# Kernel tuning notes

Measured on AMD Instinct MI355X. Metric: run time of the kernel, lower is better.

The kernel has to match this reference:

```python
import jax, jax.numpy as jnp
import numpy as np

N_HEADS = 4

def setup_inputs() -> dict:
    key = jax.random.key(0)
    ks = jax.random.split(key, 9)
    B, C, H, W = 4, 256, 64, 64
    nh, hs = N_HEADS, C // N_HEADS
    s = 0.02
    return {
        "x": jax.random.normal(ks[0], (B, C, H, W), jnp.float32),
        "wq": jax.random.normal(ks[1], (C, C), jnp.float32) * s,
        "bq": jax.random.normal(ks[2], (C,), jnp.float32) * s,
        "wk": jax.random.normal(ks[3], (C, C), jnp.float32) * s,
        "bk": jax.random.normal(ks[4], (C,), jnp.float32) * s,
        "wv": jax.random.normal(ks[5], (C, C), jnp.float32) * s,
        "bv": jax.random.normal(ks[6], (C,), jnp.float32) * s,
        "rel_h": jax.random.normal(ks[7], (1, nh, hs, 1, H), jnp.float32),
        "rel_w": jax.random.normal(ks[8], (1, nh, hs, W, 1), jnp.float32),
    }

def reference(x, wq, bq, wk, bk, wv, bv, rel_h, rel_w):
    B, C, H, W = x.shape
    nh = N_HEADS
    hs = C // nh
    S = H * W

    def proj(w, b):
        # 1x1 conv == per-pixel linear over channels -> [B, C, H, W]
        y = jnp.einsum('oc,bchw->bohw', w, x) + b[None, :, None, None]
        # faithful to torch .view: flatten [C,H,W] row-major into [S, nh, hs]
        y = y.reshape(B, S, nh, hs)
        return y.transpose(0, 2, 1, 3)  # [B, nh, S, hs]

    q = proj(wq, bq)
    k = proj(wk, bk)
    v = proj(wv, bv)

    # content scores (NOTE: no 1/sqrt(d) scaling in BoT override)
    attn_content = jnp.einsum('bnqd,bnkd->bnqk', q, k)  # [B, nh, S, S]
    # learned relative position term: broadcast-add then flatten (w,h) order
    pos = (rel_h + rel_w).reshape(1, nh, hs, S)  # [1, nh, hs, S]
    attn_position = jnp.einsum('bnqd,ands->bnqs', q, pos)  # [B, nh, S, S]

    probs = jax.nn.softmax(attn_content + attn_position, axis=-1)
    ctx = jnp.einsum('bnqk,bnkd->bnqd', probs, v)  # [B, nh, S, hs]
    # faithful to torch: transpose(1,2) then view(B, C, width, height)
    out = ctx.transpose(0, 2, 1, 3).reshape(B, C, W, H)
    return out
```

## Files before the change

kernel.cpp:

```cpp
#include <hip/hip_runtime.h>
#include <hip/hip_bf16.h>
#include <stdint.h>
#include <math.h>

typedef __bf16 bf16_t;
typedef __bf16 bf16x8 __attribute__((ext_vector_type(8)));
typedef float  f32x4  __attribute__((ext_vector_type(4)));
typedef float  f32x16 __attribute__((ext_vector_type(16)));
typedef unsigned int u32;

#define S_SZ 4096
#define HS   64
#define OUT_B_STRIDE (256 * 64 * 64)
#define LOG2E 1.4426950408889634f

#define GLOAD_LDS(gsrc, ldst)                                                              \
    __builtin_amdgcn_global_load_lds((__attribute__((address_space(1))) void*)(void*)(gsrc), \
                                     (__attribute__((address_space(3))) void*)(void*)(ldst),  \
                                     16, 0, 0)

static __device__ __forceinline__ u32 pack2(__bf16 a, __bf16 b) {
    return (u32)__builtin_bit_cast(uint16_t, a) | ((u32)__builtin_bit_cast(uint16_t, b) << 16);
}

__global__ __launch_bounds__(256)
void prep_kernel(const float* __restrict__ wq, const float* __restrict__ wk,
                 const float* __restrict__ wv, const float* __restrict__ rel_h,
                 const float* __restrict__ rel_w,
                 bf16_t* __restrict__ Wh, bf16_t* __restrict__ Wl,
                 bf16_t* __restrict__ Rt)
{
    const int blk = blockIdx.x;
    if (blk < 48) {
        const int base = blk * 4096;
        #pragma unroll
        for (int i = 0; i < 16; ++i) {
            const int e = base + i * 256 + threadIdx.x;
            const int o = e >> 8, c = e & 255;
            const float* src = o < 256 ? wq : (o < 512 ? wk : wv);
            float v = src[(size_t)(o & 255) * 256 + c];
            if (o < 256) v *= LOG2E;
            __bf16 h = (__bf16)v;
            Wh[e] = h;
            Wl[e] = (__bf16)(v - (float)h);
        }
    } else {
        const int rb = blk - 48;
        const int n = rb >> 4, h2 = rb & 15;
        __shared__ float rh[4096], rw[4096];
        for (int i = threadIdx.x; i < 4096; i += 256) {
            rh[i] = rel_h[n * 4096 + i];
            rw[i] = rel_w[n * 4096 + i];
        }
        __syncthreads();
        bf16_t* Rp = Rt + ((size_t)n * 4096 + h2 * 256) * 64;
        const int d0 = (threadIdx.x & 7) * 8;
        const int ob = threadIdx.x >> 3;
        #pragma unroll
        for (int i = 0; i < 8; ++i) {
            const int o  = i * 32 + ob;
            const int ih = (o & 3) * 16 + h2;
            const int iw = o >> 2;
            bf16x8 rv;
            #pragma unroll
            for (int dd = 0; dd < 8; ++dd)
                rv[dd] = (bf16_t)(rh[(d0 + dd) * 64 + ih] + rw[(d0 + dd) * 64 + iw]);
            *(bf16x8*)(Rp + (size_t)o * 64 + d0) = rv;
        }
    }
}

__global__ __launch_bounds__(512, 2)
void proj_kernel(const float* __restrict__ x,
                 const bf16_t* __restrict__ Wh, const bf16_t* __restrict__ Wl,
                 const float* __restrict__ bq, const float* __restrict__ bk,
                 const float* __restrict__ bv, const bf16_t* __restrict__ Rt,
                 bf16_t* __restrict__ q_ws, bf16_t* __restrict__ k2_ws,
                 bf16_t* __restrict__ vt2_ws)
{
    const int bx = blockIdx.x;
    const int b  = bx >> 6;
    const int h  = bx & 63;
    const int p0 = h * 64;
    const int n  = h & 3;
    const int h2 = h >> 2;
    const int bn = b * 4 + n;
    const int tid = threadIdx.x;

    __shared__ __align__(16) char SM[65536];

    {
        const int cpair = tid & 127, pg = tid >> 7;
        const int c0 = cpair * 2;
        const float* x0 = x + ((size_t)b * 256 + c0) * 4096 + p0 + pg * 16;
        const int sub = (c0 >> 6) * 128;
        const int u   = (c0 >> 3) & 7;
        const int e2  = (c0 & 7) * 2;
        #pragma unroll
        for (int i4 = 0; i4 < 4; ++i4) {
            f32x4 ra = *(const f32x4*)(x0 + i4 * 4);
            f32x4 rb = *(const f32x4*)(x0 + 4096 + i4 * 4);
            #pragma unroll
            for (int i = 0; i < 4; ++i) {
                const int p = pg * 16 + i4 * 4 + i;
                __bf16 ha = (__bf16)ra[i], hb = (__bf16)rb[i];
                float  la = ra[i] - (float)ha, lb = rb[i] - (float)hb;
                const int off = p * 512 + sub + ((u ^ (p & 7)) * 16) + e2;
                *(u32*)(SM + off)         = pack2(ha, hb);
                *(u32*)(SM + 32768 + off) = pack2((__bf16)la, (__bf16)lb);
            }
        }
    }
    __syncthreads();

    const int wid = tid >> 6, lane = tid & 63, l31 = lane & 31, hi = lane >> 5;

    int obs[3], pjs[3];
    const bf16_t* whp[3];
    const bf16_t* wlp[3];
    #pragma unroll
    for (int j = 0; j < 3; ++j) {
        const int of = (wid * 3 + j) * 32;
        pjs[j] = of >> 8;
        obs[j] = of & 255;
        whp[j] = Wh + (size_t)(of + l31) * 256 + hi * 8;
        wlp[j] = Wl + (size_t)(of + l31) * 256 + hi * 8;
    }

    const char* XHp = SM + l31 * 512;
    const char* XLp = SM + 32768 + l31 * 512;

    f32x16 acc[3][2] = {};

    bf16x8 whC[3], wlC[3], whN[3], wlN[3];
    #pragma unroll
    for (int j = 0; j < 3; ++j) {
        whC[j] = *(const bf16x8*)(whp[j]);
        wlC[j] = *(const bf16x8*)(wlp[j]);
    }

    #pragma unroll
    for (int ks = 0; ks < 16; ++ks) {
        if (ks < 15) {
            #pragma unroll
            for (int j = 0; j < 3; ++j) {
                whN[j] = *(const bf16x8*)(whp[j] + (ks + 1) * 16);
                wlN[j] = *(const bf16x8*)(wlp[j] + (ks + 1) * 16);
            }
        }
        const int rb_ = (ks >> 2) * 128 + ((((ks * 2 + hi) & 7) ^ (l31 & 7)) * 16);
        bf16x8 xh[2], xl[2];
        #pragma unroll
        for (int pt = 0; pt < 2; ++pt) {
            xh[pt] = *(const bf16x8*)(XHp + pt * 16384 + rb_);
            xl[pt] = *(const bf16x8*)(XLp + pt * 16384 + rb_);
        }
        #pragma unroll
        for (int j = 0; j < 3; ++j)
            #pragma unroll
            for (int pt = 0; pt < 2; ++pt) {
                acc[j][pt] = __builtin_amdgcn_mfma_f32_32x32x16_bf16(whC[j], xh[pt], acc[j][pt], 0, 0, 0);
                acc[j][pt] = __builtin_amdgcn_mfma_f32_32x32x16_bf16(whC[j], xl[pt], acc[j][pt], 0, 0, 0);
                acc[j][pt] = __builtin_amdgcn_mfma_f32_32x32x16_bf16(wlC[j], xh[pt], acc[j][pt], 0, 0, 0);
            }
        #pragma unroll
        for (int j = 0; j < 3; ++j) { whC[j] = whN[j]; wlC[j] = wlN[j]; }
    }
    __syncthreads();

    f32x4 bias[3][2][4];
    #pragma unroll
    for (int j = 0; j < 3; ++j) {
        const float* bp = pjs[j] == 0 ? bq : (pjs[j] == 1 ? bk : bv);
        #pragma unroll
        for (int g2 = 0; g2 < 4; ++g2) {
            f32x4 v = *(const f32x4*)(bp + obs[j] + hi * 4 + g2 * 8);
            if (pjs[j] == 0) {
                #pragma unroll
                for (int i = 0; i < 4; ++i) v[i] *= LOG2E;
            }
            bias[j][0][g2] = v;  bias[j][1][g2] = v;
        }
    }

    #pragma unroll
    for (int j = 0; j < 3; ++j) {
        if (pjs[j] == 1) continue;
        #pragma unroll
        for (int pt = 0; pt < 2; ++pt) {
            const int d = pt * 32 + l31;
            #pragma unroll
            for (int g2 = 0; g2 < 4; ++g2)
                #pragma unroll
                for (int rr = 0; rr < 4; ++rr) {
                    const int o = obs[j] + rr + 4 * hi + 8 * g2;
                    const float v = acc[j][pt][g2 * 4 + rr] + bias[j][pt][g2][rr];
                    if (pjs[j] == 0) {
                        *(bf16_t*)(SM + o * 128 + d * 2) = (bf16_t)v;
                    } else {
                        *(bf16_t*)(SM + 32768 + d * 512 + ((o * 2) ^ ((d & 7) << 4))) = (bf16_t)v;
                    }
                }
        }
    }
    __syncthreads();
    {
        bf16_t* qp = q_ws + (size_t)bn * 4096 * 64;
        #pragma unroll
        for (int i = 0; i < 4; ++i) {
            const int c = i * 512 + tid;
            const int o = c >> 3, d8 = c & 7;
            uint4 v = *(const uint4*)(SM + c * 16);
            *(uint4*)(qp + (size_t)(o * 16 + h2) * 64 + d8 * 8) = v;
        }
        bf16_t* vp = vt2_ws + (size_t)bn * 64 * 4096 + h2 * 256;
        #pragma unroll
        for (int i = 0; i < 4; ++i) {
            const int c = i * 512 + tid;
            const int d = c >> 5, k = c & 31;
            uint4 v = *(const uint4*)(SM + 32768 + d * 512 + ((k * 16) ^ ((d & 7) << 4)));
            *(uint4*)(vp + (size_t)d * 4096 + k * 8) = v;
        }
    }
    __syncthreads();

    #pragma unroll
    for (int j = 0; j < 3; ++j) {
        if (pjs[j] != 1) continue;
        #pragma unroll
        for (int pt = 0; pt < 2; ++pt) {
            const int d = pt * 32 + l31;
            #pragma unroll
            for (int g2 = 0; g2 < 4; ++g2)
                #pragma unroll
                for (int rr = 0; rr < 4; ++rr) {
                    const int o = obs[j] + rr + 4 * hi + 8 * g2;
                    *(bf16_t*)(SM + o * 128 + d * 2) =
                        (bf16_t)(acc[j][pt][g2 * 4 + rr] + bias[j][pt][g2][rr]);
                }
        }
    }
    __syncthreads();
    {
        const bf16_t* Rp = Rt + ((size_t)n * 4096 + h2 * 256) * 64;
        bf16_t* kp = k2_ws + ((size_t)bn * 4096 + h2 * 256) * 64;
        #pragma unroll
        for (int i = 0; i < 4; ++i) {
            const int c = i * 512 + tid;
            bf16x8 kv = *(const bf16x8*)(SM + c * 16);
            bf16x8 rv = *(const bf16x8*)(Rp + c * 8);
            bf16x8 res;
            #pragma unroll
            for (int ii = 0; ii < 8; ++ii)
                res[ii] = (__bf16)((float)kv[ii] + (float)rv[ii]);
            *(bf16x8*)(kp + c * 8) = res;
        }
    }
}

__global__ __launch_bounds__(256, 1)
void attn_kernel(const bf16_t* __restrict__ q_ws, const bf16_t* __restrict__ k_ws,
                 const bf16_t* __restrict__ vt_ws, float* __restrict__ out)
{
    const int tid  = threadIdx.x;
    const int wid  = tid >> 6;
    const int lane = tid & 63;
    const int l31  = lane & 31;
    const int hi   = lane >> 5;

    const int wg  = blockIdx.x;
    const int swz = (wg & 7) * 32 + (wg >> 3);
    const int bn  = swz >> 4;
    const int qb  = swz & 15;
    const int b   = bn >> 2, n = bn & 3;

    __shared__ __align__(16) bf16_t Kt[4][64 * 64];
    __shared__ __align__(16) bf16_t Vt[4][64 * 64];

    const bf16_t* Qb = q_ws  + (size_t)bn * S_SZ * HS;
    const bf16_t* Kb = k_ws  + (size_t)bn * S_SZ * HS;
    const bf16_t* Vb = vt_ws + (size_t)bn * HS * S_SZ;

    const int c0 = wid * 64 + lane;
    const int ra = c0 >> 3, ga = (c0 & 7) ^ (ra & 7);
    const bf16_t* ksrcA = Kb + ra * HS + ga * 8;
    const bf16_t* ksrcB = ksrcA + 32 * HS;
    const bf16_t* vsrcA = Vb + (size_t)ra * S_SZ + ga * 8;
    const bf16_t* vsrcB = vsrcA + (size_t)32 * S_SZ;

#define STAGE(buf, ts)                                                        \
    GLOAD_LDS(ksrcA + (size_t)(ts) * 64 * HS, &Kt[buf][wid * 512]);           \
    GLOAD_LDS(ksrcB + (size_t)(ts) * 64 * HS, &Kt[buf][2048 + wid * 512]);    \
    GLOAD_LDS(vsrcA + (ts) * 64,              &Vt[buf][wid * 512]);           \
    GLOAD_LDS(vsrcB + (ts) * 64,              &Vt[buf][2048 + wid * 512]);

    const int q0 = qb * 256 + wid * 64 + l31;
    bf16x8 qf0[4], qf1[4];
    #pragma unroll
    for (int dk = 0; dk < 4; ++dk) {
        qf0[dk] = *(const bf16x8*)(Qb + (size_t)q0 * HS + dk * 16 + hi * 8);
        qf1[dk] = *(const bf16x8*)(Qb + (size_t)(q0 + 32) * HS + dk * 16 + hi * 8);
    }

    f32x16 oacc[2][2];
    f32x16 Z16;
    #pragma unroll
    for (int i = 0; i < 16; ++i) {
        oacc[0][0][i] = 0.f; oacc[0][1][i] = 0.f;
        oacc[1][0][i] = 0.f; oacc[1][1][i] = 0.f;
        Z16[i] = 0.f;
    }
    float lsum0 = 0.f, lsum1 = 0.f;

    const int swzme = (l31 & 7) << 4;

#define TILE(BUF)                                                                      \
    { const char* Kb_ = (const char*)&Kt[BUF][0] + l31 * 128;                          \
      const char* Vb_ = (const char*)&Vt[BUF][0] + l31 * 128;                          \
      f32x16 sacc[2][2];                                                               \
      _Pragma("unroll")                                                                \
      for (int hh = 0; hh < 2; ++hh) {                                                 \
          bf16x8 kf[4];                                                                \
          _Pragma("unroll")                                                            \
          for (int dk = 0; dk < 4; ++dk)                                               \
              kf[dk] = *(const bf16x8*)(Kb_ + hh * 4096 + (((2 * dk + hi) * 16) ^ swzme)); \
          sacc[hh][0] = __builtin_amdgcn_mfma_f32_32x32x16_bf16(kf[0], qf0[0], Z16, 0, 0, 0); \
          sacc[hh][1] = __builtin_amdgcn_mfma_f32_32x32x16_bf16(kf[0], qf1[0], Z16, 0, 0, 0); \
          _Pragma("unroll")                                                            \
          for (int dk = 1; dk < 4; ++dk) {                                             \
              sacc[hh][0] = __builtin_amdgcn_mfma_f32_32x32x16_bf16(kf[dk], qf0[dk], sacc[hh][0], 0, 0, 0); \
              sacc[hh][1] = __builtin_amdgcn_mfma_f32_32x32x16_bf16(kf[dk], qf1[dk], sacc[hh][1], 0, 0, 0); \
          }                                                                            \
      }                                                                                \
      u32 F0[4][4], F1[4][4];                                                          \
      { u32 Wd[2][4][2];                                                               \
        float ps[4] = {0.f, 0.f, 0.f, 0.f};                                            \
        _Pragma("unroll")                                                              \
        for (int hh = 0; hh < 2; ++hh)                                                 \
        _Pragma("unroll")                                                              \
        for (int c = 0; c < 4; ++c)                                                    \
        _Pragma("unroll")                                                              \
        for (int tt = 0; tt < 2; ++tt) {                                               \
            float pa = __builtin_amdgcn_exp2f(sacc[hh][0][c * 4 + tt * 2]);            \
            float pb = __builtin_amdgcn_exp2f(sacc[hh][0][c * 4 + tt * 2 + 1]);        \
            ps[c] += pa + pb;                                                          \
            u32 w_;                                                                    \
            asm("v_cvt_pk_bf16_f32 %0, %1, %2" : "=v"(w_) : "v"(pa), "v"(pb));         \
            Wd[hh][c][tt] = w_; }                                                      \
        lsum0 += (ps[0] + ps[1]) + (ps[2] + ps[3]);                                    \
        _Pragma("unroll")                                                              \
        for (int hh = 0; hh < 2; ++hh)                                                 \
        _Pragma("unroll")                                                              \
        for (int pr = 0; pr < 2; ++pr)                                                 \
        _Pragma("unroll")                                                              \
        for (int tt = 0; tt < 2; ++tt) {                                               \
            u32 a_ = Wd[hh][2 * pr][tt], b_ = Wd[hh][2 * pr + 1][tt];                  \
            asm("v_permlane32_swap_b32 %0, %1" : "+v"(a_), "+v"(b_));                  \
            F0[2 * hh + pr][tt]     = a_;                                              \
            F0[2 * hh + pr][2 + tt] = b_; } }                                          \
      { u32 Wd[2][4][2];                                                               \
        float ps[4] = {0.f, 0.f, 0.f, 0.f};                                            \
        _Pragma("unroll")                                                              \
        for (int hh = 0; hh < 2; ++hh)                                                 \
        _Pragma("unroll")                                                              \
        for (int c = 0; c < 4; ++c)                                                    \
        _Pragma("unroll")                                                              \
        for (int tt = 0; tt < 2; ++tt) {                                               \
            float pa = __builtin_amdgcn_exp2f(sacc[hh][1][c * 4 + tt * 2]);            \
            float pb = __builtin_amdgcn_exp2f(sacc[hh][1][c * 4 + tt * 2 + 1]);        \
            ps[c] += pa + pb;                                                          \
            u32 w_;                                                                    \
            asm("v_cvt_pk_bf16_f32 %0, %1, %2" : "=v"(w_) : "v"(pa), "v"(pb));         \
            Wd[hh][c][tt] = w_; }                                                      \
        lsum1 += (ps[0] + ps[1]) + (ps[2] + ps[3]);                                    \
        _Pragma("unroll")                                                              \
        for (int hh = 0; hh < 2; ++hh)                                                 \
        _Pragma("unroll")                                                              \
        for (int pr = 0; pr < 2; ++pr)                                                 \
        _Pragma("unroll")                                                              \
        for (int tt = 0; tt < 2; ++tt) {                                               \
            u32 a_ = Wd[hh][2 * pr][tt], b_ = Wd[hh][2 * pr + 1][tt];                  \
            asm("v_permlane32_swap_b32 %0, %1" : "+v"(a_), "+v"(b_));                  \
            F1[2 * hh + pr][tt]     = a_;                                              \
            F1[2 * hh + pr][2 + tt] = b_; } }                                          \
      _Pragma("unroll")                                                                \
      for (int dh = 0; dh < 2; ++dh)                                                   \
      _Pragma("unroll")                                                                \
      for (int kk = 0; kk < 4; ++kk) {                                                 \
          bf16x8 vf = *(const bf16x8*)(Vb_ + dh * 4096 + (((2 * kk + hi) * 16) ^ swzme)); \
          union { u32 u[4]; bf16x8 v; } p0, p1;                                        \
          p0.u[0] = F0[kk][0]; p0.u[1] = F0[kk][1]; p0.u[2] = F0[kk][2]; p0.u[3] = F0[kk][3]; \
          p1.u[0] = F1[kk][0]; p1.u[1] = F1[kk][1]; p1.u[2] = F1[kk][2]; p1.u[3] = F1[kk][3]; \
          oacc[dh][0] = __builtin_amdgcn_mfma_f32_32x32x16_bf16(vf, p0.v, oacc[dh][0], 0, 0, 0); \
          oacc[dh][1] = __builtin_amdgcn_mfma_f32_32x32x16_bf16(vf, p1.v, oacc[dh][1], 0, 0, 0); } }

    STAGE(0, 0); STAGE(1, 1); STAGE(2, 2);
    asm volatile("s_waitcnt vmcnt(8)" ::: "memory");
    __builtin_amdgcn_s_barrier();
    asm volatile("" ::: "memory");

    for (int tb = 0; tb < 64; tb += 4) {
        #pragma unroll
        for (int u = 0; u < 4; ++u) {
            const int t = tb + u;
            { const int ts = (t + 3 > 63) ? 63 : t + 3; STAGE((u + 3) & 3, ts); }
            TILE(u);
            asm volatile("s_waitcnt vmcnt(4)" ::: "memory");
            __builtin_amdgcn_s_barrier();
            asm volatile("" ::: "memory");
        }
    }
#undef TILE
#undef STAGE

    float lt0 = lsum0 + __shfl_xor(lsum0, 32);
    float lt1 = lsum1 + __shfl_xor(lsum1, 32);
    float inv0 = 1.0f / lt0;
    float inv1 = 1.0f / lt1;
    float* outp0 = out + (size_t)b * OUT_B_STRIDE + (size_t)q0 * 256 + n * 64;
    float* outp1 = outp0 + 32 * 256;
    #pragma unroll
    for (int dh = 0; dh < 2; ++dh)
        #pragma unroll
        for (int g2 = 0; g2 < 4; ++g2) {
            f32x4 v4, w4;
            #pragma unroll
            for (int r = 0; r < 4; ++r) {
                v4[r] = oacc[dh][0][g2 * 4 + r] * inv0;
                w4[r] = oacc[dh][1][g2 * 4 + r] * inv1;
            }
            *(f32x4*)(outp0 + dh * 32 + g2 * 8 + hi * 4) = v4;
            *(f32x4*)(outp1 + dh * 32 + g2 * 8 + hi * 4) = w4;
        }
}

extern "C" void kernel_launch(void* const* d_in, const int* in_sizes, int n_in,
                              void* d_out, int out_size, void* d_ws, size_t ws_size,
                              hipStream_t stream)
{
    const float* x     = (const float*)d_in[0];
    const float* wq    = (const float*)d_in[1];
    const float* bq    = (const float*)d_in[2];
    const float* wk    = (const float*)d_in[3];
    const float* bk    = (const float*)d_in[4];
    const float* wv    = (const float*)d_in[5];
    const float* bv    = (const float*)d_in[6];
    const float* rel_h = (const float*)d_in[7];
    const float* rel_w = (const float*)d_in[8];
    float* out = (float*)d_out;

    bf16_t* q_ws   = (bf16_t*)d_ws;
    bf16_t* k2_ws  = q_ws  + (size_t)16 * S_SZ * HS;
    bf16_t* vt2_ws = k2_ws + (size_t)16 * S_SZ * HS;

    bf16_t* end = (bf16_t*)d_out + (size_t)out_size * 2;
    bf16_t* Wl  = end - 196608;
    bf16_t* Wh  = Wl - 196608;
    bf16_t* Rt  = Wh - 1048576;

    prep_kernel<<<112, 256, 0, stream>>>(wq, wk, wv, rel_h, rel_w, Wh, Wl, Rt);
    proj_kernel<<<256, 512, 0, stream>>>(x, Wh, Wl, bq, bk, bv, Rt,
                                         q_ws, k2_ws, vt2_ws);
    attn_kernel<<<256, 256, 0, stream>>>(q_ws, k2_ws, vt2_ws, out);
}
```

Baseline: 138.4 us.

## Split attention KV range in two halves and merge with a combine kernel

The attention kernel now splits each (batch, head, query-block) work item into two halves over the key/value sequence. This launches 512 workgroups instead of 256, with launch bounds set for two blocks per CU and the LDS staging cut from four buffers to two. Each half writes its unnormalised output and row sums to workspace, and a new elementwise combine kernel adds the halves and divides by the total sum. The aim is more waves per CU to hide latency, at the cost of a shallower prefetch pipeline, extra global traffic for partial outputs, and one more launch. The merge is only exact if the two halves share the same softmax max reference, which depends on hidden code.

```diff
diff --git a/kernel.cpp b/kernel.cpp
--- a/kernel.cpp
+++ b/kernel.cpp
@@ -258,9 +258,11 @@
     }
 }
 
-__global__ __launch_bounds__(256, 1)
+__global__ __launch_bounds__(256, 2)
 void attn_kernel(const bf16_t* __restrict__ q_ws, const bf16_t* __restrict__ k_ws,
-                 const bf16_t* __restrict__ vt_ws, float* __restrict__ out)
+                 const bf16_t* __restrict__ vt_ws, float* __restrict__ O0,
+                 float* __restrict__ L0, float* __restrict__ L1,
+                 float* __restrict__ out)
 {
     const int tid  = threadIdx.x;
     const int wid  = tid >> 6;
@@ -269,13 +271,16 @@
     const int hi   = lane >> 5;
 
     const int wg  = blockIdx.x;
-    const int swz = (wg & 7) * 32 + (wg >> 3);
-    const int bn  = swz >> 4;
-    const int qb  = swz & 15;
-    const int b   = bn >> 2, n = bn & 3;
-
-    __shared__ __align__(16) bf16_t Kt[4][64 * 64];
-    __shared__ __align__(16) bf16_t Vt[4][64 * 64];
+    const int swz = (wg & 7) * 64 + (wg >> 3);
+    const int bn  = swz >> 5;
+    const int r   = swz & 31;
+    const int qb  = r >> 1;
+    const int half = r & 1;
+    const int tbase = half * 32;
+    const int b = bn >> 2, n = bn & 3;
+
+    __shared__ __align__(16) bf16_t Kt[2][64 * 64];
+    __shared__ __align__(16) bf16_t Vt[2][64 * 64];
 
     const bf16_t* Qb = q_ws  + (size_t)bn * S_SZ * HS;
     const bf16_t* Kb = k_ws  + (size_t)bn * S_SZ * HS;
@@ -394,30 +399,29 @@
           oacc[dh][0] = __builtin_amdgcn_mfma_f32_32x32x16_bf16(vf, p0.v, oacc[dh][0], 0, 0, 0); \
           oacc[dh][1] = __builtin_amdgcn_mfma_f32_32x32x16_bf16(vf, p1.v, oacc[dh][1], 0, 0, 0); } }
 
-    STAGE(0, 0); STAGE(1, 1); STAGE(2, 2);
-    asm volatile("s_waitcnt vmcnt(8)" ::: "memory");
+    STAGE(0, tbase);
+    asm volatile("s_waitcnt vmcnt(0)" ::: "memory");
     __builtin_amdgcn_s_barrier();
     asm volatile("" ::: "memory");
-
-    for (int tb = 0; tb < 64; tb += 4) {
-        #pragma unroll
-        for (int u = 0; u < 4; ++u) {
-            const int t = tb + u;
-            { const int ts = (t + 3 > 63) ? 63 : t + 3; STAGE((u + 3) & 3, ts); }
-            TILE(u);
-            asm volatile("s_waitcnt vmcnt(4)" ::: "memory");
-            __builtin_amdgcn_s_barrier();
-            asm volatile("" ::: "memory");
-        }
+    for (int t = 0; t < 32; t += 2) {
+        { const int ts = tbase + ((t + 1 < 32) ? t + 1 : 31); STAGE(1, ts); }
+        TILE(0);
+        asm volatile("s_waitcnt vmcnt(0)" ::: "memory");
+        __builtin_amdgcn_s_barrier();
+        asm volatile("" ::: "memory");
+        { const int ts = tbase + ((t + 2 < 32) ? t + 2 : 31); STAGE(0, ts); }
+        TILE(1);
+        asm volatile("s_waitcnt vmcnt(0)" ::: "memory");
+        __builtin_amdgcn_s_barrier();
+        asm volatile("" ::: "memory");
     }
 #undef TILE
 #undef STAGE
 
     float lt0 = lsum0 + __shfl_xor(lsum0, 32);
     float lt1 = lsum1 + __shfl_xor(lsum1, 32);
-    float inv0 = 1.0f / lt0;
-    float inv1 = 1.0f / lt1;
-    float* outp0 = out + (size_t)b * OUT_B_STRIDE + (size_t)q0 * 256 + n * 64;
+    float* Otgt = half ? out : O0;
+    float* outp0 = Otgt + (size_t)b * OUT_B_STRIDE + (size_t)q0 * 256 + n * 64;
     float* outp1 = outp0 + 32 * 256;
     #pragma unroll
     for (int dh = 0; dh < 2; ++dh)
@@ -425,13 +429,42 @@
         for (int g2 = 0; g2 < 4; ++g2) {
             f32x4 v4, w4;
             #pragma unroll
-            for (int r = 0; r < 4; ++r) {
-                v4[r] = oacc[dh][0][g2 * 4 + r] * inv0;
-                w4[r] = oacc[dh][1][g2 * 4 + r] * inv1;
+            for (int r2 = 0; r2 < 4; ++r2) {
+                v4[r2] = oacc[dh][0][g2 * 4 + r2];
+                w4[r2] = oacc[dh][1][g2 * 4 + r2];
             }
             *(f32x4*)(outp0 + dh * 32 + g2 * 8 + hi * 4) = v4;
             *(f32x4*)(outp1 + dh * 32 + g2 * 8 + hi * 4) = w4;
         }
+    if (hi == 0) {
+        float* Lp = half ? L1 : L0;
+        Lp[bn * 4096 + q0]      = lt0;
+        Lp[bn * 4096 + q0 + 32] = lt1;
+    }
+}
+
+__global__ __launch_bounds__(256)
+void combine_kernel(const float* __restrict__ O0, const float* __restrict__ L0,
+                    const float* __restrict__ L1, float* __restrict__ out)
+{
+    const int i = (blockIdx.x * 256 + threadIdx.x) * 8;
+    const int s = (i >> 8) & 4095;
+    const int b = i >> 20;
+    const int n = (i >> 6) & 3;
+    const int li = (b * 4 + n) * 4096 + s;
+    const float inv = 1.0f / (L0[li] + L1[li]);
+    f32x4 a0 = *(const f32x4*)(O0 + i);
+    f32x4 a1 = *(const f32x4*)(out + i);
+    f32x4 b0 = *(const f32x4*)(O0 + i + 4);
+    f32x4 b1 = *(const f32x4*)(out + i + 4);
+    f32x4 r0, r1;
+    #pragma unroll
+    for (int k = 0; k < 4; ++k) {
+        r0[k] = (a0[k] + a1[k]) * inv;
+        r1[k] = (b0[k] + b1[k]) * inv;
+    }
+    *(f32x4*)(out + i)     = r0;
+    *(f32x4*)(out + i + 4) = r1;
 }
 
 extern "C" void kernel_launch(void* const* d_in, const int* in_sizes, int n_in,
@@ -452,6 +485,9 @@
     bf16_t* q_ws   = (bf16_t*)d_ws;
     bf16_t* k2_ws  = q_ws  + (size_t)16 * S_SZ * HS;
     bf16_t* vt2_ws = k2_ws + (size_t)16 * S_SZ * HS;
+    float*  O0     = (float*)((char*)d_ws + 25165824);
+    float*  L0     = (float*)((char*)d_ws + 41943040);
+    float*  L1     = (float*)((char*)d_ws + 42205184);
 
     bf16_t* end = (bf16_t*)d_out + (size_t)out_size * 2;
     bf16_t* Wl  = end - 196608;
@@ -461,5 +497,6 @@
     prep_kernel<<<112, 256, 0, stream>>>(wq, wk, wv, rel_h, rel_w, Wh, Wl, Rt);
     proj_kernel<<<256, 512, 0, stream>>>(x, Wh, Wl, bq, bk, bv, Rt,
                                          q_ws, k2_ws, vt2_ws);
-    attn_kernel<<<256, 256, 0, stream>>>(q_ws, k2_ws, vt2_ws, out);
+    attn_kernel<<<512, 256, 0, stream>>>(q_ws, k2_ws, vt2_ws, O0, L0, L1, out);
+    combine_kernel<<<2048, 256, 0, stream>>>(O0, L0, L1, out);
 }
```

Result: faster. 131.7 us (-4.8%).

## Split attention into 128-thread blocks with double-buffered K/V staging

Applied to the files above, without the earlier changes.

The attention kernel now runs 512 workgroups of 2 waves, each covering 128 queries instead of 256, with launch bounds allowing 2 blocks per CU. The K/V LDS ring shrinks from 4 stages to 2 and the loop waits for all loads to finish (vmcnt(0)) before each barrier. The aim is more resident workgroups and better CU balance across the 256 CUs. The cost is that each K/V tile is loaded by twice as many blocks, and the shallower pipeline exposes more load latency.

```diff
diff --git a/kernel.cpp b/kernel.cpp
--- a/kernel.cpp
+++ b/kernel.cpp
@@ -258,7 +258,7 @@
     }
 }
 
-__global__ __launch_bounds__(256, 1)
+__global__ __launch_bounds__(128, 2)
 void attn_kernel(const bf16_t* __restrict__ q_ws, const bf16_t* __restrict__ k_ws,
                  const bf16_t* __restrict__ vt_ws, float* __restrict__ out)
 {
@@ -269,32 +269,39 @@
     const int hi   = lane >> 5;
 
     const int wg  = blockIdx.x;
-    const int swz = (wg & 7) * 32 + (wg >> 3);
-    const int bn  = swz >> 4;
-    const int qb  = swz & 15;
+    const int swz = (wg & 7) * 64 + (wg >> 3);
+    const int bn  = swz >> 5;
+    const int qb  = swz & 31;
     const int b   = bn >> 2, n = bn & 3;
 
-    __shared__ __align__(16) bf16_t Kt[4][64 * 64];
-    __shared__ __align__(16) bf16_t Vt[4][64 * 64];
+    __shared__ __align__(16) bf16_t Kt[2][64 * 64];
+    __shared__ __align__(16) bf16_t Vt[2][64 * 64];
 
     const bf16_t* Qb = q_ws  + (size_t)bn * S_SZ * HS;
     const bf16_t* Kb = k_ws  + (size_t)bn * S_SZ * HS;
     const bf16_t* Vb = vt_ws + (size_t)bn * HS * S_SZ;
 
-    const int c0 = wid * 64 + lane;
-    const int ra = c0 >> 3, ga = (c0 & 7) ^ (ra & 7);
-    const bf16_t* ksrcA = Kb + ra * HS + ga * 8;
-    const bf16_t* ksrcB = ksrcA + 32 * HS;
-    const bf16_t* vsrcA = Vb + (size_t)ra * S_SZ + ga * 8;
-    const bf16_t* vsrcB = vsrcA + (size_t)32 * S_SZ;
+    const bf16_t* ksrc[4];
+    const bf16_t* vsrc[4];
+    int dstoff[4];
+    #pragma unroll
+    for (int i = 0; i < 4; ++i) {
+        const int c = wid * 64 + i * 128 + lane;
+        const int row = c >> 3, ga = (c & 7) ^ (row & 7);
+        ksrc[i] = Kb + (size_t)row * HS + ga * 8;
+        vsrc[i] = Vb + (size_t)row * S_SZ + ga * 8;
+        dstoff[i] = (wid * 64 + i * 128) * 8;
+    }
 
 #define STAGE(buf, ts)                                                        \
-    GLOAD_LDS(ksrcA + (size_t)(ts) * 64 * HS, &Kt[buf][wid * 512]);           \
-    GLOAD_LDS(ksrcB + (size_t)(ts) * 64 * HS, &Kt[buf][2048 + wid * 512]);    \
-    GLOAD_LDS(vsrcA + (ts) * 64,              &Vt[buf][wid * 512]);           \
-    GLOAD_LDS(vsrcB + (ts) * 64,              &Vt[buf][2048 + wid * 512]);
-
-    const int q0 = qb * 256 + wid * 64 + l31;
+    { _Pragma("unroll")                                                       \
+      for (int i_ = 0; i_ < 4; ++i_)                                          \
+          GLOAD_LDS(ksrc[i_] + (size_t)(ts) * 64 * HS, &Kt[buf][dstoff[i_]]); \
+      _Pragma("unroll")                                                       \
+      for (int i_ = 0; i_ < 4; ++i_)                                          \
+          GLOAD_LDS(vsrc[i_] + (ts) * 64, &Vt[buf][dstoff[i_]]); }
+
+    const int q0 = qb * 128 + wid * 64 + l31;
     bf16x8 qf0[4], qf1[4];
     #pragma unroll
     for (int dk = 0; dk < 4; ++dk) {
@@ -394,21 +401,21 @@
           oacc[dh][0] = __builtin_amdgcn_mfma_f32_32x32x16_bf16(vf, p0.v, oacc[dh][0], 0, 0, 0); \
           oacc[dh][1] = __builtin_amdgcn_mfma_f32_32x32x16_bf16(vf, p1.v, oacc[dh][1], 0, 0, 0); } }
 
-    STAGE(0, 0); STAGE(1, 1); STAGE(2, 2);
-    asm volatile("s_waitcnt vmcnt(8)" ::: "memory");
+    STAGE(0, 0);
+    asm volatile("s_waitcnt vmcnt(0)" ::: "memory");
     __builtin_amdgcn_s_barrier();
     asm volatile("" ::: "memory");
-
-    for (int tb = 0; tb < 64; tb += 4) {
-        #pragma unroll
-        for (int u = 0; u < 4; ++u) {
-            const int t = tb + u;
-            { const int ts = (t + 3 > 63) ? 63 : t + 3; STAGE((u + 3) & 3, ts); }
-            TILE(u);
-            asm volatile("s_waitcnt vmcnt(4)" ::: "memory");
-            __builtin_amdgcn_s_barrier();
-            asm volatile("" ::: "memory");
-        }
+    for (int t = 0; t < 64; t += 2) {
+        { const int ts = (t + 1 < 64) ? t + 1 : 63; STAGE(1, ts); }
+        TILE(0);
+        asm volatile("s_waitcnt vmcnt(0)" ::: "memory");
+        __builtin_amdgcn_s_barrier();
+        asm volatile("" ::: "memory");
+        { const int ts = (t + 2 < 64) ? t + 2 : 63; STAGE(0, ts); }
+        TILE(1);
+        asm volatile("s_waitcnt vmcnt(0)" ::: "memory");
+        __builtin_amdgcn_s_barrier();
+        asm volatile("" ::: "memory");
     }
 #undef TILE
 #undef STAGE
@@ -425,9 +432,9 @@
         for (int g2 = 0; g2 < 4; ++g2) {
             f32x4 v4, w4;
             #pragma unroll
-            for (int r = 0; r < 4; ++r) {
-                v4[r] = oacc[dh][0][g2 * 4 + r] * inv0;
-                w4[r] = oacc[dh][1][g2 * 4 + r] * inv1;
+            for (int r2 = 0; r2 < 4; ++r2) {
+                v4[r2] = oacc[dh][0][g2 * 4 + r2] * inv0;
+                w4[r2] = oacc[dh][1][g2 * 4 + r2] * inv1;
             }
             *(f32x4*)(outp0 + dh * 32 + g2 * 8 + hi * 4) = v4;
             *(f32x4*)(outp1 + dh * 32 + g2 * 8 + hi * 4) = w4;
@@ -461,5 +468,5 @@
     prep_kernel<<<112, 256, 0, stream>>>(wq, wk, wv, rel_h, rel_w, Wh, Wl, Rt);
     proj_kernel<<<256, 512, 0, stream>>>(x, Wh, Wl, bq, bk, bv, Rt,
                                          q_ws, k2_ws, vt2_ws);
-    attn_kernel<<<256, 256, 0, stream>>>(q_ws, k2_ws, vt2_ws, out);
+    attn_kernel<<<512, 128, 0, stream>>>(q_ws, k2_ws, vt2_ws, out);
 }
```

Result: slower. 171.8 us (+24.2%).
